# Kernel optimization log

Measured on AMD Instinct MI355X. Metric: run time of the kernel, lower is better.

Reference implementation:

```python
import jax, jax.numpy as jnp
import numpy as np

N = 20000
IN_C = 512
HID = 64
H1 = 8
OUT_C = 256
E = 320000
NEG_SLOPE = 0.2


def gat_conv(x, src, dst, W, a_src, a_dst, b, concat):
    # PyG GATConv (shared lin for src/dst), inference mode (no dropout).
    H, C = a_src.shape
    h = (x @ W).reshape(N, H, C)                      # [N,H,C]
    alpha_src = (h * a_src[None]).sum(-1)             # [N,H]
    alpha_dst = (h * a_dst[None]).sum(-1)             # [N,H]
    alpha = jax.nn.leaky_relu(alpha_src[src] + alpha_dst[dst], NEG_SLOPE)  # [E,H]
    # segment softmax over incoming edges of each dst node
    amax = jax.ops.segment_max(alpha, dst, num_segments=N)
    amax = jnp.where(jnp.isfinite(amax), amax, 0.0)
    ex = jnp.exp(alpha - amax[dst])
    denom = jax.ops.segment_sum(ex, dst, num_segments=N)
    coef = ex / (denom[dst] + 1e-16)                  # [E,H]
    msg = h[src] * coef[:, :, None]                   # [E,H,C]
    out = jax.ops.segment_sum(msg, dst, num_segments=N)  # [N,H,C]
    out = out.reshape(N, H * C) if concat else out.mean(axis=1)
    return out + b


def setup_inputs() -> dict:
    key = jax.random.key(0)
    ks = jax.random.split(key, 10)
    x = jax.random.normal(ks[0], (N, IN_C), dtype=jnp.float32)
    edge_index = jax.random.randint(ks[1], (2, E), 0, N, dtype=jnp.int32)
    s1 = 1.0 / np.sqrt(IN_C)
    s2 = 1.0 / np.sqrt(HID * H1)
    W1 = jax.random.uniform(ks[2], (IN_C, H1 * HID), jnp.float32, -s1, s1)
    att_src1 = jax.random.uniform(ks[3], (H1, HID), jnp.float32, -s1, s1)
    att_dst1 = jax.random.uniform(ks[4], (H1, HID), jnp.float32, -s1, s1)
    b1 = jnp.zeros((H1 * HID,), jnp.float32)
    W2 = jax.random.uniform(ks[5], (H1 * HID, OUT_C), jnp.float32, -s2, s2)
    att_src2 = jax.random.uniform(ks[6], (1, OUT_C), jnp.float32, -s2, s2)
    att_dst2 = jax.random.uniform(ks[7], (1, OUT_C), jnp.float32, -s2, s2)
    b2 = jnp.zeros((OUT_C,), jnp.float32)
    return {"x": x, "edge_index": edge_index, "W1": W1, "att_src1": att_src1,
            "att_dst1": att_dst1, "b1": b1, "W2": W2, "att_src2": att_src2,
            "att_dst2": att_dst2, "b2": b2}


def reference(x, edge_index, W1, att_src1, att_dst1, b1, W2, att_src2, att_dst2, b2):
    # add self-loops (PyG GATConv default add_self_loops=True)
    loop = jnp.arange(N, dtype=edge_index.dtype)
    src = jnp.concatenate([edge_index[0], loop])
    dst = jnp.concatenate([edge_index[1], loop])
    h = gat_conv(x, src, dst, W1, att_src1, att_dst1, b1, concat=True)
    h = jax.nn.elu(h)
    out = gat_conv(h, src, dst, W2, att_src2, att_dst2, b2, concat=False)
    return jax.nn.log_softmax(out, axis=1)
```

## Files before the change

### kernel.cpp

```cpp
#include <hip/hip_runtime.h>
#include <math.h>

#define N_NODES 20000
#define NP1     20001
#define IN_CH   512
#define HID_TOT 512
#define OUT_CH  256
#define N_EDGE  320000
#define TOT_EDGE (N_EDGE + N_NODES)
#define EPAD    400000
#define NSEG    ((N_NODES + 255) / 256)

typedef __attribute__((ext_vector_type(8))) short short8;
typedef __attribute__((ext_vector_type(4))) float f32x4;
typedef __attribute__((ext_vector_type(2))) float f32x2;

__device__ __forceinline__ ushort f2bf(float f) {
    union { float f; unsigned u; } v; v.f = f;
    unsigned u = v.u;
    return (ushort)((u + 0x7fffu + ((u >> 16) & 1u)) >> 16);
}

__device__ __forceinline__ void glds16(const ushort* g, ushort* l) {
    __builtin_amdgcn_global_load_lds(
        (const __attribute__((address_space(1))) void*)g,
        (__attribute__((address_space(3))) void*)l, 16, 0, 0);
}

__device__ __forceinline__ float lrelu(float a) { return fmaxf(a, 0.2f * a); }

#define NA_BLK (N_NODES * IN_CH / 4 / 256)
#define NB_BLK ((IN_CH / 64) * (HID_TOT / 4))
#define NC_BLK ((HID_TOT / 64) * (OUT_CH / 4))
#define NZ_BLK ((N_NODES + 255) / 256)
__global__ __launch_bounds__(256) void prep_kernel(const float* __restrict__ x,
                                                   ushort* __restrict__ xb,
                                                   const float* __restrict__ W1,
                                                   ushort* __restrict__ w1t,
                                                   const float* __restrict__ W2,
                                                   ushort* __restrict__ w2t,
                                                   int* __restrict__ counts,
                                                   float* __restrict__ as1,
                                                   float* __restrict__ as2,
                                                   float* __restrict__ ad2,
                                                   unsigned char* __restrict__ h1f,
                                                   unsigned char* __restrict__ h2f) {
    int b = blockIdx.x;
    int t = threadIdx.x;
    if (b < NA_BLK) {
        int i = b * 256 + t;
        float4 v = *(const float4*)&x[(size_t)i * 4];
        ushort4 o = make_ushort4(f2bf(v.x), f2bf(v.y), f2bf(v.z), f2bf(v.w));
        *(ushort4*)&xb[(size_t)i * 4] = o;
    } else if (b < NA_BLK + NB_BLK) {
        int bb = b - NA_BLK;
        int k = (bb & 7) * 64 + (t & 63);
        int n = (bb >> 3) * 4 + (t >> 6);
        w1t[(size_t)n * IN_CH + k] = f2bf(W1[(size_t)k * HID_TOT + n]);
    } else if (b < NA_BLK + NB_BLK + NC_BLK) {
        int bb = b - NA_BLK - NB_BLK;
        int k = (bb & 7) * 64 + (t & 63);
        int n = (bb >> 3) * 4 + (t >> 6);
        w2t[(size_t)n * HID_TOT + k] = f2bf(W2[(size_t)k * OUT_CH + n]);
    } else {
        int i = (b - NA_BLK - NB_BLK - NC_BLK) * 256 + t;
        if (i < N_NODES) { counts[i] = 0; as2[i] = 0.f; ad2[i] = 0.f; }
        if (i == N_NODES) as2[N_NODES] = -1e30f;
        if (i < 8) as1[(size_t)i * NP1 + N_NODES] = -1e30f;
        if (i < 128)
            ((unsigned*)(h1f + ((size_t)(i >> 4) * NP1 + N_NODES) * 64))[i & 15] = 0u;
        if (i < 64)
            ((unsigned*)(h2f + (size_t)N_NODES * OUT_CH))[i] = 0u;
    }
}

__global__ void hist_kernel(const int* __restrict__ ei, int* __restrict__ counts) {
    int e = blockIdx.x * blockDim.x + threadIdx.x;
    if (e >= TOT_EDGE) return;
    int d = (e < N_EDGE) ? ei[N_EDGE + e] : (e - N_EDGE);
    atomicAdd(&counts[d], 1);
}

__global__ __launch_bounds__(256) void perm_kernel(const int* __restrict__ counts,
                                                   int* __restrict__ perm,
                                                   int* __restrict__ invperm,
                                                   int* __restrict__ pcnt) {
    __shared__ int bins[64], starts[64];
    int seg = blockIdx.x;
    int t = threadIdx.x;
    int v = seg * 256 + t;
    bool valid = (v < N_NODES);
    if (t < 64) bins[t] = 0;
    __syncthreads();
    int dreal = 0, d = 0, rank = 0;
    if (valid) {
        dreal = counts[v];
        d = dreal; if (d > 63) d = 63;
        rank = atomicAdd(&bins[d], 1);
    }
    __syncthreads();
    if (t == 0) {
        int r = 0;
        for (int k = 0; k < 64; k++) { starts[k] = r; r += bins[k]; }
    }
    __syncthreads();
    if (valid) {
        int pos = seg * 256 + starts[d] + rank;
        perm[pos] = v;
        invperm[v] = pos;
        pcnt[pos] = dreal;
    }
}

__global__ __launch_bounds__(1024) void scan_kernel(const int* __restrict__ pcnt,
                                                    int* __restrict__ offsets,
                                                    int* __restrict__ cursors) {
    const int C = (N_NODES + 1023) / 1024;
    int t = threadIdx.x;
    int lane = t & 63, wid = t >> 6;
    int base = t * C;
    int cnt[C];
    int sum = 0;
#pragma unroll
    for (int i = 0; i < C; i++) {
        int idx = base + i;
        cnt[i] = (idx < N_NODES) ? pcnt[idx] : 0;
        sum += (cnt[i] + 3) & ~3;
    }
    int val = sum;
#pragma unroll
    for (int off = 1; off < 64; off <<= 1) {
        int y = __shfl_up(val, off);
        if (lane >= off) val += y;
    }
    __shared__ int wsum[16], woff[16], stotal;
    if (lane == 63) wsum[wid] = val;
    __syncthreads();
    if (t == 0) {
        int r = 0;
        for (int w = 0; w < 16; w++) { woff[w] = r; r += wsum[w]; }
        stotal = r;
    }
    __syncthreads();
    int running = woff[wid] + (val - sum);
#pragma unroll
    for (int i = 0; i < C; i++) {
        int idx = base + i;
        if (idx < N_NODES) {
            offsets[idx] = running;
            cursors[idx] = running;
            running += (cnt[i] + 3) & ~3;
        }
    }
    if (t == 0) offsets[N_NODES] = stotal;
}

__global__ void scatter_kernel(const int* __restrict__ ei, const int* __restrict__ invperm,
                               const int* __restrict__ pcnt, const int* __restrict__ offsets,
                               int* __restrict__ cursors, ushort* __restrict__ srcs) {
    int idx = blockIdx.x * blockDim.x + threadIdx.x;
    if (idx < TOT_EDGE) {
        int s, d;
        if (idx < N_EDGE) { s = ei[idx]; d = ei[N_EDGE + idx]; } else { s = idx - N_EDGE; d = s; }
        int dr = invperm[d];
        int pos = atomicAdd(&cursors[dr], 1);
        srcs[pos] = (ushort)invperm[s];
    } else {
        int rk = idx - TOT_EDGE;
        if (rk < N_NODES) {
            int o = offsets[rk] + pcnt[rk], e = offsets[rk + 1];
            for (int pp = o; pp < e; pp++) srcs[pp] = (ushort)N_NODES;
        }
    }
}

__global__ __launch_bounds__(256, 2) void gemm_mfma_kernel(const ushort* __restrict__ A,
                                                           const ushort* __restrict__ Bt,
                                                           unsigned char* __restrict__ Cf8,
                                                           const float* __restrict__ asrc,
                                                           const float* __restrict__ adst,
                                                           float* __restrict__ as_out,
                                                           float* __restrict__ ad_out,
                                                           const int* __restrict__ invp,
                                                           int M, int N, int K,
                                                           int layer1, int aHM, int nbxl) {
    __shared__ ushort As[128 * 64];
    __shared__ ushort Bs[128 * 64];
    int total = gridDim.x;
    int q8 = total >> 3, r8 = total & 7;
    int xcd = blockIdx.x & 7, within = blockIdx.x >> 3;
    int l = (xcd < r8 ? xcd * (q8 + 1) : r8 * (q8 + 1) + (xcd - r8) * q8) + within;
    int bx = l & ((1 << nbxl) - 1);
    int by = l >> nbxl;

    int t = threadIdx.x;
    int lane = t & 63;
    int wave = t >> 6;
    int wr = (wave >> 1) * 64;
    int wc = (wave & 1) * 64;
    int bm = by * 128, bn = bx * 128;
    int q = lane >> 4, l15 = lane & 15;
    size_t kmul = aHM ? (size_t)NP1 : 1;

    const ushort* Aptr[4]; ushort* Alds[4];
    const ushort* Bptr[4]; ushort* Blds[4];
#pragma unroll
    for (int k = 0; k < 4; k++) {
        int c = t + 256 * k;
        int r = c >> 3, kqs = c & 7;
        int kqg = kqs ^ (r & 7);
        int ar = bm + r; if (ar >= M) ar = M - 1;
        Aptr[k] = aHM ? (A + (size_t)ar * 64 + kqg * 8)
                      : (A + (size_t)ar * K + kqg * 8);
        Alds[k] = &As[c * 8];
        Bptr[k] = Bt + (size_t)(bn + r) * K + kqg * 8;
        Blds[k] = &Bs[c * 8];
    }

    f32x4 acc[4][4];
#pragma unroll
    for (int i = 0; i < 4; i++)
#pragma unroll
        for (int j = 0; j < 4; j++) acc[i][j] = f32x4{0.f, 0.f, 0.f, 0.f};

    for (int k0 = 0; k0 < K; k0 += 64) {
        __syncthreads();
        glds16(Aptr[0] + (size_t)k0 * kmul, Alds[0]);
        glds16(Aptr[1] + (size_t)k0 * kmul, Alds[1]);
        glds16(Aptr[2] + (size_t)k0 * kmul, Alds[2]);
        glds16(Aptr[3] + (size_t)k0 * kmul, Alds[3]);
        glds16(Bptr[0] + k0, Blds[0]);
        glds16(Bptr[1] + k0, Blds[1]);
        glds16(Bptr[2] + k0, Blds[2]);
        glds16(Bptr[3] + k0, Blds[3]);
        __syncthreads();

#pragma unroll
        for (int s = 0; s < 2; s++) {
            int kq = s * 4 + q;
            short8 af[4], bf[4];
#pragma unroll
            for (int i = 0; i < 4; i++) {
                int row = wr + i * 16 + l15;
                int slot = kq ^ (row & 7);
                af[i] = *(const short8*)&As[row * 64 + slot * 8];
            }
#pragma unroll
            for (int j = 0; j < 4; j++) {
                int row = wc + j * 16 + l15;
                int slot = kq ^ (row & 7);
                bf[j] = *(const short8*)&Bs[row * 64 + slot * 8];
            }
#pragma unroll
            for (int i = 0; i < 4; i++)
#pragma unroll
                for (int j = 0; j < 4; j++)
                    acc[i][j] = __builtin_amdgcn_mfma_f32_16x16x32_bf16(af[i], bf[j], acc[i][j], 0, 0, 0);
        }
    }

    float av[4], dv[4];
#pragma unroll
    for (int j = 0; j < 4; j++) {
        int cg = bn + wc + j * 16 + l15;
        av[j] = asrc[cg];
        dv[j] = adst[cg];
    }
    float ps[4][4], pd[4][4];
#pragma unroll
    for (int i = 0; i < 4; i++)
#pragma unroll
        for (int r = 0; r < 4; r++) {
            float p = 0.f, d = 0.f;
#pragma unroll
            for (int j = 0; j < 4; j++) {
                p = fmaf(acc[i][j][r], av[j], p);
                d = fmaf(acc[i][j][r], dv[j], d);
            }
            ps[i][r] = p; pd[i][r] = d;
        }
#pragma unroll
    for (int off = 1; off < 16; off <<= 1) {
#pragma unroll
        for (int i = 0; i < 4; i++)
#pragma unroll
            for (int r = 0; r < 4; r++) {
                ps[i][r] += __shfl_xor(ps[i][r], off);
                pd[i][r] += __shfl_xor(pd[i][r], off);
            }
    }

    int hidx = bx * 2 + (wave & 1);
#pragma unroll
    for (int i = 0; i < 4; i++) {
#pragma unroll
        for (int r = 0; r < 4; r++) {
            int rg = bm + wr + i * 16 + q * 4 + r;
            if (rg < M) {
                if (layer1) {
                    int rr = invp[rg];
#pragma unroll
                    for (int j = 0; j < 4; j++) {
                        int w8 = __builtin_amdgcn_cvt_pk_fp8_f32(acc[i][j][r], acc[i][j][r], 0, false);
                        Cf8[((size_t)hidx * NP1 + rr) * 64 + j * 16 + l15] = (unsigned char)(w8 & 0xff);
                    }
                    if (l15 == 0) {
                        as_out[(size_t)hidx * NP1 + rr] = ps[i][r];
                        ad_out[(size_t)hidx * NP1 + rr] = pd[i][r];
                    }
                } else {
#pragma unroll
                    for (int j = 0; j < 4; j++) {
                        int cg = bn + wc + j * 16 + l15;
                        int w8 = __builtin_amdgcn_cvt_pk_fp8_f32(acc[i][j][r], acc[i][j][r], 0, false);
                        Cf8[(size_t)rg * N + cg] = (unsigned char)(w8 & 0xff);
                    }
                    if (l15 == 0) {
                        atomicAdd(&as_out[rg], ps[i][r]);
                        atomicAdd(&ad_out[rg], pd[i][r]);
                    }
                }
            }
        }
    }
}

__global__ __launch_bounds__(64) void agg1_kernel(const unsigned char* __restrict__ h1f,
                                                  const float* __restrict__ as1,
                                                  const float* __restrict__ ad1,
                                                  const int* __restrict__ offsets,
                                                  const ushort* __restrict__ srcs,
                                                  const float* __restrict__ b1,
                                                  ushort* __restrict__ h1ab) {
    int b = blockIdx.x;
    int head = b & 7;
    int grp = b >> 3;
    int lane = threadIdx.x;
    int sub = lane >> 3;
    int l8 = lane & 7;
    int rk = grp * 8 + sub;
    int cofs = head * 64 + l8 * 8;
    const unsigned char* hb = h1f + (size_t)head * NP1 * 64 + l8 * 8;
    const float* as1h = as1 + (size_t)head * NP1;
    float adv = ad1[(size_t)head * NP1 + rk];
    int s = offsets[rk], e = offsets[rk + 1];

    float denom = 0.f;
    float acc[8];
#pragma unroll
    for (int k = 0; k < 8; k++) acc[k] = 0.f;

    int i = s;
    uint2 ca = {0u, 0u}, cb = {0u, 0u};
    int csn = N_NODES;
    if (i + 8 <= e) {
        ca = *(const uint2*)&srcs[i];
        cb = *(const uint2*)&srcs[i + 4];
        csn = srcs[i + l8];
    }
    while (i + 8 <= e) {
        int sn[8] = {(int)(ca.x & 0xffff), (int)(ca.x >> 16),
                     (int)(ca.y & 0xffff), (int)(ca.y >> 16),
                     (int)(cb.x & 0xffff), (int)(cb.x >> 16),
                     (int)(cb.y & 0xffff), (int)(cb.y >> 16)};
        uint2 r[8];
#pragma unroll
        for (int j = 0; j < 8; j++)
            r[j] = *(const uint2*)&hb[(size_t)sn[j] * 64];
        float aown = as1h[csn];
        int ni = i + 8;
        uint2 na = ca, nb = cb; int nsn = csn;
        if (ni + 8 <= e) {
            na = *(const uint2*)&srcs[ni];
            nb = *(const uint2*)&srcs[ni + 4];
            nsn = srcs[ni + l8];
        }
        float w_own = __expf(lrelu(aown + adv));
        denom += w_own;
        float ww[8];
#pragma unroll
        for (int j = 0; j < 8; j++) ww[j] = __shfl(w_own, (lane & 56) | j);
#pragma unroll
        for (int j = 0; j < 8; j++) {
            f32x2 pa = __builtin_amdgcn_cvt_pk_f32_fp8(r[j].x, false);
            f32x2 pb = __builtin_amdgcn_cvt_pk_f32_fp8(r[j].x, true);
            f32x2 pc = __builtin_amdgcn_cvt_pk_f32_fp8(r[j].y, false);
            f32x2 pdd = __builtin_amdgcn_cvt_pk_f32_fp8(r[j].y, true);
            acc[0] = fmaf(ww[j], pa.x, acc[0]); acc[1] = fmaf(ww[j], pa.y, acc[1]);
            acc[2] = fmaf(ww[j], pb.x, acc[2]); acc[3] = fmaf(ww[j], pb.y, acc[3]);
            acc[4] = fmaf(ww[j], pc.x, acc[4]); acc[5] = fmaf(ww[j], pc.y, acc[5]);
            acc[6] = fmaf(ww[j], pdd.x, acc[6]); acc[7] = fmaf(ww[j], pdd.y, acc[7]);
        }
        ca = na; cb = nb; csn = nsn; i = ni;
    }
    if (i < e) {
        uint2 pa4 = *(const uint2*)&srcs[i];
        int sn[4] = {(int)(pa4.x & 0xffff), (int)(pa4.x >> 16),
                     (int)(pa4.y & 0xffff), (int)(pa4.y >> 16)};
        int snt = srcs[i + (l8 & 3)];
        uint2 r[4];
#pragma unroll
        for (int j = 0; j < 4; j++)
            r[j] = *(const uint2*)&hb[(size_t)sn[j] * 64];
        float w_own = __expf(lrelu(as1h[snt] + adv));
        if (l8 < 4) denom += w_own;
        float ww[4];
#pragma unroll
        for (int j = 0; j < 4; j++) ww[j] = __shfl(w_own, (lane & 56) | j);
#pragma unroll
        for (int j = 0; j < 4; j++) {
            f32x2 pa = __builtin_amdgcn_cvt_pk_f32_fp8(r[j].x, false);
            f32x2 pb = __builtin_amdgcn_cvt_pk_f32_fp8(r[j].x, true);
            f32x2 pc = __builtin_amdgcn_cvt_pk_f32_fp8(r[j].y, false);
            f32x2 pdd = __builtin_amdgcn_cvt_pk_f32_fp8(r[j].y, true);
            acc[0] = fmaf(ww[j], pa.x, acc[0]); acc[1] = fmaf(ww[j], pa.y, acc[1]);
            acc[2] = fmaf(ww[j], pb.x, acc[2]); acc[3] = fmaf(ww[j], pb.y, acc[3]);
            acc[4] = fmaf(ww[j], pc.x, acc[4]); acc[5] = fmaf(ww[j], pc.y, acc[5]);
            acc[6] = fmaf(ww[j], pdd.x, acc[6]); acc[7] = fmaf(ww[j], pdd.y, acc[7]);
        }
    }

    denom += __shfl_xor(denom, 1);
    denom += __shfl_xor(denom, 2);
    denom += __shfl_xor(denom, 4);

    float inv = 1.f / (denom + 1e-16f);
    short8 ov;
#pragma unroll
    for (int k = 0; k < 8; k++) {
        float o = acc[k] * inv + b1[cofs + k];
        o = (o > 0.f) ? o : expm1f(o);
        ov[k] = (short)f2bf(o);
    }
    *(short8*)&h1ab[((size_t)head * NP1 + rk) * 64 + l8 * 8] = ov;
}

__global__ __launch_bounds__(64) void agg2_kernel(const unsigned char* __restrict__ h2f,
                                                  const float* __restrict__ as2,
                                                  const float* __restrict__ ad2,
                                                  const int* __restrict__ offsets,
                                                  const ushort* __restrict__ srcs,
                                                  const int* __restrict__ perm,
                                                  const float* __restrict__ b2,
                                                  float* __restrict__ out) {
    int lane = threadIdx.x;
    int sub = lane >> 5;
    int l32 = lane & 31;
    int rk = blockIdx.x * 2 + sub;
    int c8 = l32 * 8;
    const unsigned char* hb = h2f + c8;
    float adv = ad2[rk];
    int s = offsets[rk], e = offsets[rk + 1];

    float denom = 0.f;
    float acc[8];
#pragma unroll
    for (int k = 0; k < 8; k++) acc[k] = 0.f;

    int i = s;
    uint2 ca = {0u, 0u}, cb = {0u, 0u};
    int csn = N_NODES;
    if (i + 8 <= e) {
        ca = *(const uint2*)&srcs[i];
        cb = *(const uint2*)&srcs[i + 4];
        csn = srcs[i + (l32 & 7)];
    }
    while (i + 8 <= e) {
        int sn[8] = {(int)(ca.x & 0xffff), (int)(ca.x >> 16),
                     (int)(ca.y & 0xffff), (int)(ca.y >> 16),
                     (int)(cb.x & 0xffff), (int)(cb.x >> 16),
                     (int)(cb.y & 0xffff), (int)(cb.y >> 16)};
        uint2 r[8];
#pragma unroll
        for (int j = 0; j < 8; j++)
            r[j] = *(const uint2*)&hb[(size_t)sn[j] * OUT_CH];
        float aown = as2[csn];
        int ni = i + 8;
        uint2 na = ca, nb = cb; int nsn = csn;
        if (ni + 8 <= e) {
            na = *(const uint2*)&srcs[ni];
            nb = *(const uint2*)&srcs[ni + 4];
            nsn = srcs[ni + (l32 & 7)];
        }
        float w_own = __expf(lrelu(aown + adv));
        if (l32 < 8) denom += w_own;
        float ww[8];
#pragma unroll
        for (int j = 0; j < 8; j++) ww[j] = __shfl(w_own, (lane & 32) | j);
#pragma unroll
        for (int j = 0; j < 8; j++) {
            f32x2 pa = __builtin_amdgcn_cvt_pk_f32_fp8(r[j].x, false);
            f32x2 pb = __builtin_amdgcn_cvt_pk_f32_fp8(r[j].x, true);
            f32x2 pc = __builtin_amdgcn_cvt_pk_f32_fp8(r[j].y, false);
            f32x2 pdd = __builtin_amdgcn_cvt_pk_f32_fp8(r[j].y, true);
            acc[0] = fmaf(ww[j], pa.x, acc[0]); acc[1] = fmaf(ww[j], pa.y, acc[1]);
            acc[2] = fmaf(ww[j], pb.x, acc[2]); acc[3] = fmaf(ww[j], pb.y, acc[3]);
            acc[4] = fmaf(ww[j], pc.x, acc[4]); acc[5] = fmaf(ww[j], pc.y, acc[5]);
            acc[6] = fmaf(ww[j], pdd.x, acc[6]); acc[7] = fmaf(ww[j], pdd.y, acc[7]);
        }
        ca = na; cb = nb; csn = nsn; i = ni;
    }
    if (i < e) {
        uint2 pa4 = *(const uint2*)&srcs[i];
        int sn[4] = {(int)(pa4.x & 0xffff), (int)(pa4.x >> 16),
                     (int)(pa4.y & 0xffff), (int)(pa4.y >> 16)};
        int snt = srcs[i + (l32 & 3)];
        uint2 r[4];
#pragma unroll
        for (int j = 0; j < 4; j++)
            r[j] = *(const uint2*)&hb[(size_t)sn[j] * OUT_CH];
        float w_own = __expf(lrelu(as2[snt] + adv));
        if (l32 < 4) denom += w_own;
        float ww[4];
#pragma unroll
        for (int j = 0; j < 4; j++) ww[j] = __shfl(w_own, (lane & 32) | j);
#pragma unroll
        for (int j = 0; j < 4; j++) {
            f32x2 pa = __builtin_amdgcn_cvt_pk_f32_fp8(r[j].x, false);
            f32x2 pb = __builtin_amdgcn_cvt_pk_f32_fp8(r[j].x, true);
            f32x2 pc = __builtin_amdgcn_cvt_pk_f32_fp8(r[j].y, false);
            f32x2 pdd = __builtin_amdgcn_cvt_pk_f32_fp8(r[j].y, true);
            acc[0] = fmaf(ww[j], pa.x, acc[0]); acc[1] = fmaf(ww[j], pa.y, acc[1]);
            acc[2] = fmaf(ww[j], pb.x, acc[2]); acc[3] = fmaf(ww[j], pb.y, acc[3]);
            acc[4] = fmaf(ww[j], pc.x, acc[4]); acc[5] = fmaf(ww[j], pc.y, acc[5]);
            acc[6] = fmaf(ww[j], pdd.x, acc[6]); acc[7] = fmaf(ww[j], pdd.y, acc[7]);
        }
    }

    denom += __shfl_xor(denom, 1);
    denom += __shfl_xor(denom, 2);
    denom += __shfl_xor(denom, 4);
    denom += __shfl_xor(denom, 8);
    denom += __shfl_xor(denom, 16);

    float inv = 1.f / (denom + 1e-16f);
    float xv[8];
#pragma unroll
    for (int k = 0; k < 8; k++) xv[k] = acc[k] * inv + b2[c8 + k];

    float mm = xv[0];
#pragma unroll
    for (int k = 1; k < 8; k++) mm = fmaxf(mm, xv[k]);
#pragma unroll
    for (int off = 1; off < 32; off <<= 1) mm = fmaxf(mm, __shfl_xor(mm, off));
    float sum = 0.f;
#pragma unroll
    for (int k = 0; k < 8; k++) sum += __expf(xv[k] - mm);
#pragma unroll
    for (int off = 1; off < 32; off <<= 1) sum += __shfl_xor(sum, off);
    float ls = logf(sum);
    int vorig = perm[rk];
    float4 o0, o1;
    o0.x = xv[0] - mm - ls; o0.y = xv[1] - mm - ls;
    o0.z = xv[2] - mm - ls; o0.w = xv[3] - mm - ls;
    o1.x = xv[4] - mm - ls; o1.y = xv[5] - mm - ls;
    o1.z = xv[6] - mm - ls; o1.w = xv[7] - mm - ls;
    *(float4*)&out[(size_t)vorig * OUT_CH + c8] = o0;
    *(float4*)&out[(size_t)vorig * OUT_CH + c8 + 4] = o1;
}

static inline size_t align256(size_t x) { return (x + 255) & ~(size_t)255; }

extern "C" void kernel_launch(void* const* d_in, const int* in_sizes, int n_in,
                              void* d_out, int out_size, void* d_ws, size_t ws_size,
                              hipStream_t stream) {
    const float* x    = (const float*)d_in[0];
    const int*   ei   = (const int*)d_in[1];
    const float* W1   = (const float*)d_in[2];
    const float* as1w = (const float*)d_in[3];
    const float* ad1w = (const float*)d_in[4];
    const float* b1   = (const float*)d_in[5];
    const float* W2   = (const float*)d_in[6];
    const float* as2w = (const float*)d_in[7];
    const float* ad2w = (const float*)d_in[8];
    const float* b2   = (const float*)d_in[9];
    float* out = (float*)d_out;

    char* p = (char*)d_ws;
    unsigned char* h1f = (unsigned char*)p; p += align256((size_t)8 * NP1 * 64);
    unsigned char* h2f = (unsigned char*)p; p += align256((size_t)NP1 * OUT_CH);
    ushort* xb   = (ushort*)p; p += align256(sizeof(ushort) * (size_t)8 * NP1 * 64);
    ushort* h1ab = xb;
    ushort* w1t  = (ushort*)p; p += align256(sizeof(ushort) * (size_t)IN_CH * HID_TOT);
    ushort* w2t  = (ushort*)p; p += align256(sizeof(ushort) * (size_t)HID_TOT * OUT_CH);
    float* as1  = (float*)p; p += align256(sizeof(float) * (size_t)NP1 * 8);
    float* ad1  = (float*)p; p += align256(sizeof(float) * (size_t)NP1 * 8);
    float* as2  = (float*)p; p += align256(sizeof(float) * (size_t)NP1);
    float* ad2  = (float*)p; p += align256(sizeof(float) * (size_t)NP1);
    int* counts  = (int*)p; p += align256(sizeof(int) * (size_t)N_NODES);
    int* offsets = (int*)p; p += align256(sizeof(int) * (size_t)(N_NODES + 1));
    int* cursors = (int*)p; p += align256(sizeof(int) * (size_t)N_NODES);
    int* perm    = (int*)p; p += align256(sizeof(int) * (size_t)N_NODES);
    int* invperm = (int*)p; p += align256(sizeof(int) * (size_t)N_NODES);
    int* pcnt    = (int*)p; p += align256(sizeof(int) * (size_t)N_NODES);
    ushort* srcs = (ushort*)p; p += align256(sizeof(ushort) * (size_t)EPAD);

    prep_kernel<<<NA_BLK + NB_BLK + NC_BLK + NZ_BLK, 256, 0, stream>>>(
        x, xb, W1, w1t, W2, w2t, counts, as1, as2, ad2, h1f, h2f);

    int eb = (TOT_EDGE + 255) / 256;
    hist_kernel<<<eb, 256, 0, stream>>>(ei, counts);
    perm_kernel<<<NSEG, 256, 0, stream>>>(counts, perm, invperm, pcnt);
    scan_kernel<<<1, 1024, 0, stream>>>(pcnt, offsets, cursors);
    int sb = (TOT_EDGE + N_NODES + 255) / 256;
    scatter_kernel<<<sb, 256, 0, stream>>>(ei, invperm, pcnt, offsets, cursors, srcs);

    int g1 = (HID_TOT / 128) * ((N_NODES + 127) / 128);
    gemm_mfma_kernel<<<g1, 256, 0, stream>>>(
        xb, w1t, h1f, as1w, ad1w, as1, ad1, invperm, N_NODES, HID_TOT, IN_CH, 1, 0, 2);
    agg1_kernel<<<2500 * 8, 64, 0, stream>>>(h1f, as1, ad1, offsets, srcs, b1, h1ab);

    int g2 = (OUT_CH / 128) * ((N_NODES + 127) / 128);
    gemm_mfma_kernel<<<g2, 256, 0, stream>>>(
        h1ab, w2t, h2f, as2w, ad2w, as2, ad2, invperm, N_NODES, OUT_CH, HID_TOT, 0, 1, 1);
    agg2_kernel<<<N_NODES / 2, 64, 0, stream>>>(h2f, as2, ad2, offsets, srcs, perm, b2, out);
}
```

Baseline: 254.8 us.

## Fuse CSR build into one cooperative kernel with grid syncs

Replaces the four CSR construction kernels (histogram, degree-sorted permutation, scan, scatter) with a single cooperative kernel that uses grid-wide syncs between phases. The single-block scan becomes a per-segment partial sum, a serial prefix over segment totals, and a parallel per-segment scan. This removes several kernel launch gaps and the serial 1024-thread scan, at the cost of grid.sync overhead and capping the grid at 512 blocks. It also swaps expm1f and logf for the faster __expf-1 and __logf intrinsics, which are less precise.

```diff
diff --git a/kernel.cpp b/kernel.cpp
--- a/kernel.cpp
+++ b/kernel.cpp
@@ -1,5 +1,8 @@
 #include <hip/hip_runtime.h>
+#include <hip/hip_cooperative_groups.h>
 #include <math.h>
+
+namespace cg = cooperative_groups;
 
 #define N_NODES 20000
 #define NP1     20001
@@ -10,6 +13,7 @@
 #define TOT_EDGE (N_EDGE + N_NODES)
 #define EPAD    400000
 #define NSEG    ((N_NODES + 255) / 256)
+#define CSR_BLOCKS 512
 
 typedef __attribute__((ext_vector_type(8))) short short8;
 typedef __attribute__((ext_vector_type(4))) float f32x4;
@@ -74,103 +78,101 @@
     }
 }
 
-__global__ void hist_kernel(const int* __restrict__ ei, int* __restrict__ counts) {
-    int e = blockIdx.x * blockDim.x + threadIdx.x;
-    if (e >= TOT_EDGE) return;
-    int d = (e < N_EDGE) ? ei[N_EDGE + e] : (e - N_EDGE);
-    atomicAdd(&counts[d], 1);
-}
-
-__global__ __launch_bounds__(256) void perm_kernel(const int* __restrict__ counts,
-                                                   int* __restrict__ perm,
-                                                   int* __restrict__ invperm,
-                                                   int* __restrict__ pcnt) {
-    __shared__ int bins[64], starts[64];
-    int seg = blockIdx.x;
+__global__ __launch_bounds__(256) void csr_kernel(const int* __restrict__ ei,
+                                                  int* __restrict__ counts,
+                                                  int* __restrict__ perm,
+                                                  int* __restrict__ invperm,
+                                                  int* __restrict__ pcnt,
+                                                  int* __restrict__ segpre,
+                                                  int* __restrict__ offsets,
+                                                  int* __restrict__ cursors,
+                                                  ushort* __restrict__ srcs) {
+    cg::grid_group grid = cg::this_grid();
     int t = threadIdx.x;
-    int v = seg * 256 + t;
-    bool valid = (v < N_NODES);
-    if (t < 64) bins[t] = 0;
-    __syncthreads();
-    int dreal = 0, d = 0, rank = 0;
-    if (valid) {
-        dreal = counts[v];
-        d = dreal; if (d > 63) d = 63;
-        rank = atomicAdd(&bins[d], 1);
-    }
-    __syncthreads();
-    if (t == 0) {
+    int gtid = blockIdx.x * 256 + t;
+    int gstride = gridDim.x * 256;
+    __shared__ int bins[64], starts[64], redsum[4], wsum[4], woff[4];
+
+    for (int e = gtid; e < TOT_EDGE; e += gstride) {
+        int d = (e < N_EDGE) ? ei[N_EDGE + e] : (e - N_EDGE);
+        atomicAdd(&counts[d], 1);
+    }
+    grid.sync();
+
+    for (int seg = blockIdx.x; seg < NSEG; seg += gridDim.x) {
+        int v = seg * 256 + t;
+        bool valid = (v < N_NODES);
+        if (t < 64) bins[t] = 0;
+        __syncthreads();
+        int dreal = 0, d = 0, rank = 0;
+        if (valid) {
+            dreal = counts[v];
+            d = dreal; if (d > 63) d = 63;
+            rank = atomicAdd(&bins[d], 1);
+        }
+        __syncthreads();
+        if (t == 0) {
+            int r = 0;
+            for (int k = 0; k < 64; k++) { starts[k] = r; r += bins[k]; }
+        }
+        __syncthreads();
+        if (valid) {
+            int pos = seg * 256 + starts[d] + rank;
+            perm[pos] = v;
+            invperm[v] = pos;
+            pcnt[pos] = dreal;
+        }
+        int pad = valid ? ((dreal + 3) & ~3) : 0;
+#pragma unroll
+        for (int off = 1; off < 64; off <<= 1) pad += __shfl_xor(pad, off);
+        if ((t & 63) == 0) redsum[t >> 6] = pad;
+        __syncthreads();
+        if (t == 0) segpre[seg] = redsum[0] + redsum[1] + redsum[2] + redsum[3];
+        __syncthreads();
+    }
+    grid.sync();
+
+    if (blockIdx.x == 0 && t == 0) {
         int r = 0;
-        for (int k = 0; k < 64; k++) { starts[k] = r; r += bins[k]; }
-    }
-    __syncthreads();
-    if (valid) {
-        int pos = seg * 256 + starts[d] + rank;
-        perm[pos] = v;
-        invperm[v] = pos;
-        pcnt[pos] = dreal;
-    }
-}
-
-__global__ __launch_bounds__(1024) void scan_kernel(const int* __restrict__ pcnt,
-                                                    int* __restrict__ offsets,
-                                                    int* __restrict__ cursors) {
-    const int C = (N_NODES + 1023) / 1024;
-    int t = threadIdx.x;
-    int lane = t & 63, wid = t >> 6;
-    int base = t * C;
-    int cnt[C];
-    int sum = 0;
-#pragma unroll
-    for (int i = 0; i < C; i++) {
-        int idx = base + i;
-        cnt[i] = (idx < N_NODES) ? pcnt[idx] : 0;
-        sum += (cnt[i] + 3) & ~3;
-    }
-    int val = sum;
-#pragma unroll
-    for (int off = 1; off < 64; off <<= 1) {
-        int y = __shfl_up(val, off);
-        if (lane >= off) val += y;
-    }
-    __shared__ int wsum[16], woff[16], stotal;
-    if (lane == 63) wsum[wid] = val;
-    __syncthreads();
-    if (t == 0) {
-        int r = 0;
-        for (int w = 0; w < 16; w++) { woff[w] = r; r += wsum[w]; }
-        stotal = r;
-    }
-    __syncthreads();
-    int running = woff[wid] + (val - sum);
-#pragma unroll
-    for (int i = 0; i < C; i++) {
-        int idx = base + i;
-        if (idx < N_NODES) {
-            offsets[idx] = running;
-            cursors[idx] = running;
-            running += (cnt[i] + 3) & ~3;
-        }
-    }
-    if (t == 0) offsets[N_NODES] = stotal;
-}
-
-__global__ void scatter_kernel(const int* __restrict__ ei, const int* __restrict__ invperm,
-                               const int* __restrict__ pcnt, const int* __restrict__ offsets,
-                               int* __restrict__ cursors, ushort* __restrict__ srcs) {
-    int idx = blockIdx.x * blockDim.x + threadIdx.x;
-    if (idx < TOT_EDGE) {
+        for (int s2 = 0; s2 < NSEG; s2++) { int c = segpre[s2]; segpre[s2] = r; r += c; }
+        offsets[N_NODES] = r;
+    }
+    grid.sync();
+
+    for (int seg = blockIdx.x; seg < NSEG; seg += gridDim.x) {
+        int idx = seg * 256 + t;
+        int cnt = (idx < N_NODES) ? pcnt[idx] : 0;
+        int pad = (cnt + 3) & ~3;
+        int lane = t & 63, wid = t >> 6;
+        int val = pad;
+#pragma unroll
+        for (int off = 1; off < 64; off <<= 1) {
+            int y = __shfl_up(val, off);
+            if (lane >= off) val += y;
+        }
+        if (lane == 63) wsum[wid] = val;
+        __syncthreads();
+        if (t == 0) {
+            int r = 0;
+            for (int w = 0; w < 4; w++) { woff[w] = r; r += wsum[w]; }
+        }
+        __syncthreads();
+        int excl = segpre[seg] + woff[wid] + (val - pad);
+        if (idx < N_NODES) { offsets[idx] = excl; cursors[idx] = excl; }
+        __syncthreads();
+    }
+    grid.sync();
+
+    for (int e = gtid; e < TOT_EDGE; e += gstride) {
         int s, d;
-        if (idx < N_EDGE) { s = ei[idx]; d = ei[N_EDGE + idx]; } else { s = idx - N_EDGE; d = s; }
+        if (e < N_EDGE) { s = ei[e]; d = ei[N_EDGE + e]; } else { s = e - N_EDGE; d = s; }
         int dr = invperm[d];
         int pos = atomicAdd(&cursors[dr], 1);
         srcs[pos] = (ushort)invperm[s];
-    } else {
-        int rk = idx - TOT_EDGE;
-        if (rk < N_NODES) {
-            int o = offsets[rk] + pcnt[rk], e = offsets[rk + 1];
-            for (int pp = o; pp < e; pp++) srcs[pp] = (ushort)N_NODES;
-        }
+    }
+    for (int rk = gtid; rk < N_NODES; rk += gstride) {
+        int o = offsets[rk] + pcnt[rk], e2 = offsets[rk + 1];
+        for (int pp = o; pp < e2; pp++) srcs[pp] = (ushort)N_NODES;
     }
 }
 
@@ -429,7 +431,7 @@
 #pragma unroll
     for (int k = 0; k < 8; k++) {
         float o = acc[k] * inv + b1[cofs + k];
-        o = (o > 0.f) ? o : expm1f(o);
+        o = (o > 0.f) ? o : (__expf(o) - 1.f);
         ov[k] = (short)f2bf(o);
     }
     *(short8*)&h1ab[((size_t)head * NP1 + rk) * 64 + l8 * 8] = ov;
@@ -548,7 +550,7 @@
     for (int k = 0; k < 8; k++) sum += __expf(xv[k] - mm);
 #pragma unroll
     for (int off = 1; off < 32; off <<= 1) sum += __shfl_xor(sum, off);
-    float ls = logf(sum);
+    float ls = __logf(sum);
     int vorig = perm[rk];
     float4 o0, o1;
     o0.x = xv[0] - mm - ls; o0.y = xv[1] - mm - ls;
@@ -593,17 +595,17 @@
     int* perm    = (int*)p; p += align256(sizeof(int) * (size_t)N_NODES);
     int* invperm = (int*)p; p += align256(sizeof(int) * (size_t)N_NODES);
     int* pcnt    = (int*)p; p += align256(sizeof(int) * (size_t)N_NODES);
+    int* segpre  = (int*)p; p += align256(sizeof(int) * (size_t)NSEG);
     ushort* srcs = (ushort*)p; p += align256(sizeof(ushort) * (size_t)EPAD);
 
     prep_kernel<<<NA_BLK + NB_BLK + NC_BLK + NZ_BLK, 256, 0, stream>>>(
         x, xb, W1, w1t, W2, w2t, counts, as1, as2, ad2, h1f, h2f);
 
-    int eb = (TOT_EDGE + 255) / 256;
-    hist_kernel<<<eb, 256, 0, stream>>>(ei, counts);
-    perm_kernel<<<NSEG, 256, 0, stream>>>(counts, perm, invperm, pcnt);
-    scan_kernel<<<1, 1024, 0, stream>>>(pcnt, offsets, cursors);
-    int sb = (TOT_EDGE + N_NODES + 255) / 256;
-    scatter_kernel<<<sb, 256, 0, stream>>>(ei, invperm, pcnt, offsets, cursors, srcs);
+    void* cargs[] = {(void*)&ei, (void*)&counts, (void*)&perm, (void*)&invperm,
+                     (void*)&pcnt, (void*)&segpre, (void*)&offsets, (void*)&cursors,
+                     (void*)&srcs};
+    hipLaunchCooperativeKernel((void*)csr_kernel, dim3(CSR_BLOCKS), dim3(256),
+                               cargs, 0, stream);
 
     int g1 = (HID_TOT / 128) * ((N_NODES + 127) / 128);
     gemm_mfma_kernel<<<g1, 256, 0, stream>>>(
```

Measured after the change: 454.3 us. 1.78x slower.
